# Kernel tuning notes

Measured on AMD Instinct MI355X. Metric: run time of the kernel, lower is better.

The kernel has to match this reference:

```python
import jax, jax.numpy as jnp
import numpy as np
import math

B, L, D, H, R = 2, 1024, 768, 12, 256
DH = D // H  # 64


def layernorm(x, g, b, eps=1e-5):
    mu = jnp.mean(x, axis=-1, keepdims=True)
    var = jnp.mean((x - mu) ** 2, axis=-1, keepdims=True)
    return (x - mu) / jnp.sqrt(var + eps) * g + b


def setup_inputs() -> dict:
    key = jax.random.key(0)
    ks = jax.random.split(key, 8)
    x = jax.random.normal(ks[0], (B, L, D), dtype=jnp.float32)
    conv_w = jax.random.normal(ks[1], (D, 3), dtype=jnp.float32) * 0.3   # depthwise k=3
    conv_b = jnp.zeros((D,), jnp.float32)
    ln_g = jnp.ones((D,), jnp.float32)
    ln_b = jnp.zeros((D,), jnp.float32)
    qkv_w = jax.random.normal(ks[2], (3 * D, D), dtype=jnp.float32) / math.sqrt(D)
    qkv_b = jnp.zeros((3 * D,), jnp.float32)
    bn_w1 = jax.random.normal(ks[3], (R, D), dtype=jnp.float32) / math.sqrt(D)
    bn_w2 = jax.random.normal(ks[4], (H * 5, R), dtype=jnp.float32) / math.sqrt(R)
    temperature = jnp.ones((1,), jnp.float32) * 0.5
    proj_w = jax.random.normal(ks[5], (D, D), dtype=jnp.float32) / math.sqrt(D)
    proj_b = jnp.zeros((D,), jnp.float32)
    mn_g = jnp.ones((DH,), jnp.float32)
    mn_b = jnp.zeros((DH,), jnp.float32)
    return {"x": x, "conv_w": conv_w, "conv_b": conv_b, "ln_g": ln_g, "ln_b": ln_b,
            "qkv_w": qkv_w, "qkv_b": qkv_b, "bn_w1": bn_w1, "bn_w2": bn_w2,
            "temperature": temperature, "proj_w": proj_w, "proj_b": proj_b,
            "mn_g": mn_g, "mn_b": mn_b}


def reference(x, conv_w, conv_b, ln_g, ln_b, qkv_w, qkv_b, bn_w1, bn_w2,
              temperature, proj_w, proj_b, mn_g, mn_b):
    Bx, Lx, Dx = x.shape
    # causal depthwise conv1d (kernel 3, pad 2 then drop last 2 == left-pad 2)
    xp = jnp.pad(x, ((0, 0), (2, 0), (0, 0)))
    conv = (xp[:, 0:Lx] * conv_w[:, 0] + xp[:, 1:Lx + 1] * conv_w[:, 1]
            + xp[:, 2:Lx + 2] * conv_w[:, 2]) + conv_b
    x_conv = x + conv
    xn = layernorm(x_conv, ln_g, ln_b)

    qkv = xn @ qkv_w.T + qkv_b
    q, k, v = jnp.split(qkv, 3, axis=-1)

    params = (jax.nn.silu(xn @ bn_w1.T) @ bn_w2.T).reshape(Bx, Lx, H, 5)
    sem_amp = jax.nn.sigmoid(params[..., 0])
    sem_phase = jnp.tanh(params[..., 1]) * math.pi
    ctx_amp = jax.nn.sigmoid(params[..., 2])
    ctx_phase = jnp.tanh(params[..., 3]) * math.pi
    decay = 0.3 + 0.65 * jax.nn.sigmoid(params[..., 4])  # (B,L,H)
    gate = jax.nn.sigmoid(sem_amp * ctx_amp * jnp.cos(sem_phase - ctx_phase) * temperature[0])

    q_f = (jax.nn.elu(q) + 1.0).reshape(Bx, Lx, H, DH)
    k_f = (jax.nn.elu(k) + 1.0).reshape(Bx, Lx, H, DH)
    v_f = v.reshape(Bx, Lx, H, DH)

    one_minus = 1.0 - decay                                    # (B,L,H)
    kv_input = jnp.einsum('blhd,blhe->blhde', k_f, v_f)        # (B,L,H,dh,dh)
    kv_input = jnp.clip(kv_input * (gate * one_minus)[..., None, None], -5.0, 5.0)

    df = jnp.exp(jnp.cumsum(jnp.log(decay), axis=1))           # (B,L,H)
    safe_df = df + 1e-8
    kv_states = jnp.cumsum(kv_input / safe_df[..., None, None], axis=1) * df[..., None, None]

    z = jnp.cumsum(k_f * one_minus[..., None] / safe_df[..., None], axis=1) * df[..., None]
    z = jnp.clip(z, -10000.0, 10000.0)

    out_num = jnp.einsum('blhd,blhde->blhe', q_f, kv_states)   # (B,L,H,dh)
    den = jnp.sum(q_f * z, axis=-1, keepdims=True) + 0.0001
    out = layernorm(out_num / den, mn_g, mn_b)                 # (B,L,H,dh)

    y = out.reshape(Bx, Lx, Dx) @ proj_w.T + proj_b
    return y, gate
```

## Files before the change

kernel.cpp:

```cpp
#include <hip/hip_runtime.h>
#include <math.h>

#define LL 1024
#define DD 768
#define HH 12
#define CL 16
#define NC 64
#define NBH 24

typedef __bf16 bf16x8 __attribute__((ext_vector_type(8)));
typedef __bf16 bf16x4 __attribute__((ext_vector_type(4)));
typedef float floatx4 __attribute__((ext_vector_type(4)));

typedef const void __attribute__((address_space(1)))* gas_ptr;
typedef void __attribute__((address_space(3)))* las_ptr;

__device__ __forceinline__ void gl_lds16(const void* g, void* s) {
  __builtin_amdgcn_global_load_lds((gas_ptr)g, (las_ptr)s, 16, 0, 0);
}

__device__ __forceinline__ float wave_sum64(float v) {
#pragma unroll
  for (int off = 32; off; off >>= 1) v += __shfl_xor(v, off, 64);
  return v;
}

__device__ __forceinline__ float sigm(float x) { return 1.0f / (1.0f + expf(-x)); }

__global__ __launch_bounds__(256) void convert_all(
    const float* __restrict__ qkvw, const float* __restrict__ bnw1,
    const float* __restrict__ projw, const float* __restrict__ w2,
    __bf16* __restrict__ dq, __bf16* __restrict__ d1,
    __bf16* __restrict__ dp, __bf16* __restrict__ dw2) {
  int i = blockIdx.x * 256 + threadIdx.x;
  if (i >= 647168) return;
  if (i >= 638976) {
    int off = i - 638976;
    bf16x4 o;
    if (off < 3840) {
      float4 v = ((const float4*)w2)[off];
      o[0] = (__bf16)v.x; o[1] = (__bf16)v.y; o[2] = (__bf16)v.z; o[3] = (__bf16)v.w;
    } else {
      o[0] = (__bf16)0.f; o[1] = (__bf16)0.f; o[2] = (__bf16)0.f; o[3] = (__bf16)0.f;
    }
    ((bf16x4*)dw2)[off] = o;
    return;
  }
  const float* s; __bf16* d; int off;
  if (i < 442368)      { s = qkvw;  d = dq; off = i; }
  else if (i < 491520) { s = bnw1;  d = d1; off = i - 442368; }
  else                 { s = projw; d = dp; off = i - 491520; }
  float4 v = ((const float4*)s)[off];
  bf16x4 o;
  o[0] = (__bf16)v.x; o[1] = (__bf16)v.y; o[2] = (__bf16)v.z; o[3] = (__bf16)v.w;
  ((bf16x4*)d)[off] = o;
}

__global__ __launch_bounds__(256) void conv_ln_kernel(
    const float* __restrict__ x, const float* __restrict__ cw,
    const float* __restrict__ cb, const float* __restrict__ g,
    const float* __restrict__ bta, __bf16* __restrict__ xn) {
  int row = blockIdx.x;
  int l = row & (LL - 1);
  const float* xr = x + (size_t)row * DD;
  __shared__ float red[16];
  float vals[3];
  float s = 0.f, ss = 0.f;
#pragma unroll
  for (int i = 0; i < 3; i++) {
    int d = threadIdx.x + i * 256;
    float x0 = xr[d];
    float xm1 = (l >= 1) ? xr[d - DD] : 0.f;
    float xm2 = (l >= 2) ? xr[d - 2 * DD] : 0.f;
    float c = xm2 * cw[d * 3 + 0] + xm1 * cw[d * 3 + 1] + x0 * cw[d * 3 + 2] + cb[d];
    float v = x0 + c;
    vals[i] = v; s += v; ss += v * v;
  }
  s = wave_sum64(s); ss = wave_sum64(ss);
  int wid = threadIdx.x >> 6;
  if ((threadIdx.x & 63) == 0) { red[wid * 2] = s; red[wid * 2 + 1] = ss; }
  __syncthreads();
  if (threadIdx.x == 0) {
    red[8] = red[0] + red[2] + red[4] + red[6];
    red[9] = red[1] + red[3] + red[5] + red[7];
  }
  __syncthreads();
  float mu = red[8] * (1.f / 768.f);
  float var = red[9] * (1.f / 768.f) - mu * mu;
  float inv = rsqrtf(var + 1e-5f);
  __bf16* xo = xn + (size_t)row * DD;
#pragma unroll
  for (int i = 0; i < 3; i++) {
    int d = threadIdx.x + i * 256;
    xo[d] = (__bf16)((vals[i] - mu) * inv * g[d] + bta[d]);
  }
}

template <int BM, int MODE, bool HASBIAS, bool OUTBF>
__global__ __launch_bounds__(256) void gemm_mfma_kernel(
    const __bf16* __restrict__ A, const __bf16* __restrict__ Bw,
    const float* __restrict__ bias, void* __restrict__ Cv,
    int M, int N, int K) {
  constexpr int MI = BM / 32;
  __shared__ __attribute__((aligned(16))) __bf16 As[BM * 64];
  __shared__ __attribute__((aligned(16))) __bf16 Bs[128 * 64];
  int m0 = blockIdx.y * BM, n0 = blockIdx.x * 128;
  int tid = threadIdx.x;
  int w = tid >> 6, lane = tid & 63;
  int wm = w >> 1, wn = w & 1;
  int quad = lane >> 4, l16 = lane & 15;

  int lrow = lane >> 3;
  int lchunk = (lane & 7) ^ lrow;
  int R0 = w * 8;

  floatx4 acc[MI][4];
#pragma unroll
  for (int i = 0; i < MI; i++)
#pragma unroll
    for (int j = 0; j < 4; j++) acc[i][j] = (floatx4)0.f;

  for (int k0 = 0; k0 < K; k0 += 64) {
    __syncthreads();
#pragma unroll
    for (int r = 0; r < BM / 32; r++) {
      int row = r * 32 + R0 + lrow;
      gl_lds16(A + (size_t)(m0 + row) * K + k0 + lchunk * 8, &As[(r * 32 + R0) * 64]);
    }
#pragma unroll
    for (int r = 0; r < 4; r++) {
      int row = r * 32 + R0 + lrow;
      gl_lds16(Bw + (size_t)(n0 + row) * K + k0 + lchunk * 8, &Bs[(r * 32 + R0) * 64]);
    }
    __syncthreads();
#pragma unroll
    for (int s = 0; s < 2; s++) {
      bf16x8 af[MI], bfr[4];
      int csw = (s << 2) + quad;
#pragma unroll
      for (int i = 0; i < MI; i++) {
        int m = wm * (BM / 2) + i * 16 + l16;
        af[i] = *(const bf16x8*)&As[m * 64 + (csw ^ (l16 & 7)) * 8];
      }
#pragma unroll
      for (int j = 0; j < 4; j++) {
        int n = wn * 64 + j * 16 + l16;
        bfr[j] = *(const bf16x8*)&Bs[n * 64 + (csw ^ (l16 & 7)) * 8];
      }
#pragma unroll
      for (int i = 0; i < MI; i++)
#pragma unroll
        for (int j = 0; j < 4; j++)
          acc[i][j] = __builtin_amdgcn_mfma_f32_16x16x32_bf16(af[i], bfr[j], acc[i][j], 0, 0, 0);
    }
  }
#pragma unroll
  for (int j = 0; j < 4; j++) {
    int gcol = n0 + wn * 64 + j * 16 + l16;
    float bv = HASBIAS ? bias[gcol] : 0.f;
#pragma unroll
    for (int i = 0; i < MI; i++) {
      int grow = m0 + wm * (BM / 2) + i * 16 + quad * 4;
#pragma unroll
      for (int r = 0; r < 4; r++) {
        float v = acc[i][j][r] + bv;
        if (MODE == 1) { if (gcol < 1536) v = (v > 0.f) ? v + 1.f : expf(v); }
        if (MODE == 2) { v = v / (1.f + expf(-v)); }
        if (OUTBF) ((__bf16*)Cv)[(size_t)(grow + r) * N + gcol] = (__bf16)v;
        else       ((float*)Cv)[(size_t)(grow + r) * N + gcol] = v;
      }
    }
  }
}

__global__ __launch_bounds__(256) void params_df_kernel(
    const float* __restrict__ pp, const float* __restrict__ temp,
    float* __restrict__ gate, float* __restrict__ dec, float* __restrict__ dfb) {
  int bh = blockIdx.x;
  int b = bh / HH, h = bh - b * HH;
  int tid = threadIdx.x;
  int lane = tid & 63, wid = tid >> 6;
  float tv = temp[0];
  const float PI = 3.14159265358979323846f;
  double ls[4];
  double lsum = 0.0;
#pragma unroll
  for (int i = 0; i < 4; i++) {
    int l = tid * 4 + i;
    int row = (b << 10) + l;
    const float* p = pp + (size_t)row * 128 + h * 5;
    float p0 = p[0], p1 = p[1], p2 = p[2], p3 = p[3], p4 = p[4];
    float sa = sigm(p0);
    float sp = tanhf(p1) * PI;
    float ca = sigm(p2);
    float cp = tanhf(p3) * PI;
    float dc = 0.3f + 0.65f * sigm(p4);
    float gt = sigm(sa * ca * cosf(sp - cp) * tv);
    gate[row * HH + h] = gt;
    dec[(bh << 10) + l] = dc;
    lsum += (double)logf(dc);
    ls[i] = lsum;
  }
  double run = lsum;
#pragma unroll
  for (int off = 1; off < 64; off <<= 1) {
    double n = __shfl_up(run, off, 64);
    if (lane >= off) run += n;
  }
  __shared__ double wsum[4];
  if (lane == 63) wsum[wid] = run;
  __syncthreads();
  double wexcl = 0.0;
  for (int k = 0; k < wid; k++) wexcl += wsum[k];
  double excl = wexcl + run - lsum;
  float* dfo = dfb + (bh << 10) + tid * 4;
#pragma unroll
  for (int i = 0; i < 4; i++) dfo[i] = expf((float)(excl + ls[i]));
}

__global__ __launch_bounds__(256) void scan_phase1(
    const float* __restrict__ qkv, const float* __restrict__ dec,
    const float* __restrict__ df, const float* __restrict__ gate,
    float* __restrict__ kvcs, float* __restrict__ zcs, float* __restrict__ Aarr) {
  int blk = blockIdx.x;
  int bh = blk >> 6, c = blk & (NC - 1);
  int b = bh / HH, h = bh - b * HH;
  int tid = threadIdx.x;
  int w = tid >> 6, e = tid & 63;
  int t0 = c * CL;
  __shared__ __attribute__((aligned(16))) float kbuf[CL][64];
  __shared__ __attribute__((aligned(16))) float vbuf[CL][64];
  __shared__ float sbuf[CL][4];
  const float* base = qkv + ((size_t)(b * LL + t0)) * 2304 + h * 64;
  {
    int t = (w << 2) + (e >> 4);
    int col = (e & 15) << 2;
    gl_lds16(base + (size_t)t * 2304 + 768 + col, &kbuf[w << 2][0]);
    gl_lds16(base + (size_t)t * 2304 + 1536 + col, &vbuf[w << 2][0]);
  }
  if (tid < CL) {
    int t = t0 + tid;
    float a = dec[bh * LL + t];
    float d = df[bh * LL + t];
    float r = d / (d + 1e-8f);
    float g = gate[(b * LL + t) * HH + h];
    sbuf[tid][0] = a; sbuf[tid][1] = r; sbuf[tid][2] = g * (1.f - a);
    sbuf[tid][3] = (1.f - a) * r;
  }
  __syncthreads();
  float KV[16];
#pragma unroll
  for (int d = 0; d < 16; d++) KV[d] = 0.f;
  float z = 0.f, A = 1.f;
  for (int t = 0; t < CL; t++) {
    float a = sbuf[t][0], r = sbuf[t][1], cs = sbuf[t][2], w1r = sbuf[t][3];
    float vc = vbuf[t][e] * cs;
    A *= a;
#pragma unroll
    for (int d4 = 0; d4 < 4; d4++) {
      float4 k4 = *(const float4*)&kbuf[t][(w << 4) + (d4 << 2)];
      float kr[4] = {k4.x, k4.y, k4.z, k4.w};
#pragma unroll
      for (int j = 0; j < 4; j++) {
        float u = fminf(fmaxf(kr[j] * vc, -5.f), 5.f);
        KV[(d4 << 2) + j] = fmaf(a, KV[(d4 << 2) + j], r * u);
      }
    }
    z = fmaf(a, z, kbuf[t][e] * w1r);
  }
  float* kvo = kvcs + (size_t)blk * 4096 + (w << 4) * 64 + e;
#pragma unroll
  for (int d = 0; d < 16; d++) kvo[d * 64] = KV[d];
  if (w == 0) zcs[blk * 64 + e] = z;
  if (tid == 0) Aarr[blk] = A;
}

__global__ __launch_bounds__(256) void combine_kernel(
    const float* __restrict__ Aarr, float* __restrict__ kv, float* __restrict__ z) {
  int g = blockIdx.x * 256 + threadIdx.x;
  if (g < NBH * 4096) {
    int bh = g >> 12, idx = g & 4095;
    const float* Ap = Aarr + bh * NC;
    float* p = kv + (size_t)bh * NC * 4096 + idx;
    float carry = 0.f;
#pragma unroll 8
    for (int c = 0; c < NC; c++) {
      float endv = p[(size_t)c * 4096];
      p[(size_t)c * 4096] = carry;
      carry = fmaf(Ap[c], carry, endv);
    }
  } else {
    int g2 = g - NBH * 4096;
    int bh = g2 >> 6, idx = g2 & 63;
    const float* Ap = Aarr + bh * NC;
    float* p = z + bh * NC * 64 + idx;
    float carry = 0.f;
#pragma unroll 8
    for (int c = 0; c < NC; c++) {
      float endv = p[c * 64];
      p[c * 64] = carry;
      carry = fmaf(Ap[c], carry, endv);
    }
  }
}

__global__ __launch_bounds__(256) void scan_phase3(
    const float* __restrict__ qkv, const float* __restrict__ dec,
    const float* __restrict__ df, const float* __restrict__ gate,
    const float* __restrict__ kvcs, const float* __restrict__ zcs,
    const float* __restrict__ mng, const float* __restrict__ mnb,
    __bf16* __restrict__ att) {
  int blk = blockIdx.x;
  int bh = blk >> 6, c = blk & (NC - 1);
  int b = bh / HH, h = bh - b * HH;
  int tid = threadIdx.x;
  int w = tid >> 6, e = tid & 63;
  int t0 = c * CL;
  __shared__ __attribute__((aligned(16))) float qbuf[CL][64];
  __shared__ __attribute__((aligned(16))) float kbuf[CL][64];
  __shared__ __attribute__((aligned(16))) float vbuf[CL][64];
  __shared__ float sbuf[CL][4];
  __shared__ float pbuf[CL][4][64];
  const float* base = qkv + ((size_t)(b * LL + t0)) * 2304 + h * 64;
  {
    int t = (w << 2) + (e >> 4);
    int col = (e & 15) << 2;
    gl_lds16(base + (size_t)t * 2304 + col, &qbuf[w << 2][0]);
    gl_lds16(base + (size_t)t * 2304 + 768 + col, &kbuf[w << 2][0]);
    gl_lds16(base + (size_t)t * 2304 + 1536 + col, &vbuf[w << 2][0]);
  }
  if (tid < CL) {
    int t = t0 + tid;
    float a = dec[bh * LL + t];
    float d = df[bh * LL + t];
    float r = d / (d + 1e-8f);
    float g = gate[(b * LL + t) * HH + h];
    sbuf[tid][0] = a; sbuf[tid][1] = r; sbuf[tid][2] = g * (1.f - a);
    sbuf[tid][3] = (1.f - a) * r;
  }
  float KV[16];
  const float* kvi = kvcs + (size_t)blk * 4096 + (w << 4) * 64 + e;
#pragma unroll
  for (int d = 0; d < 16; d++) KV[d] = kvi[d * 64];
  float z = zcs[blk * 64 + e];
  float zsnap[4];
  __syncthreads();
  for (int t = 0; t < CL; t++) {
    float a = sbuf[t][0], r = sbuf[t][1], cs = sbuf[t][2], w1r = sbuf[t][3];
    float vc = vbuf[t][e] * cs;
    float onp = 0.f;
#pragma unroll
    for (int d4 = 0; d4 < 4; d4++) {
      float4 k4 = *(const float4*)&kbuf[t][(w << 4) + (d4 << 2)];
      float4 q4 = *(const float4*)&qbuf[t][(w << 4) + (d4 << 2)];
      float kr[4] = {k4.x, k4.y, k4.z, k4.w};
      float qr[4] = {q4.x, q4.y, q4.z, q4.w};
#pragma unroll
      for (int j = 0; j < 4; j++) {
        float u = fminf(fmaxf(kr[j] * vc, -5.f), 5.f);
        float nv = fmaf(a, KV[(d4 << 2) + j], r * u);
        KV[(d4 << 2) + j] = nv;
        onp = fmaf(qr[j], nv, onp);
      }
    }
    pbuf[t][w][e] = onp;
    z = fmaf(a, z, kbuf[t][e] * w1r);
    if ((t >> 2) == w) zsnap[t & 3] = z;
  }
  __syncthreads();
  float mg = mng[e], mb = mnb[e];
#pragma unroll
  for (int i = 0; i < 4; i++) {
    int t = (w << 2) + i;
    float on = pbuf[t][0][e] + pbuf[t][1][e] + pbuf[t][2][e] + pbuf[t][3][e];
    float zc = fminf(fmaxf(zsnap[i], -10000.f), 10000.f);
    float qe = qbuf[t][e];
    float s0 = qe * zc, s1 = on, s2 = on * on;
#pragma unroll
    for (int off = 32; off; off >>= 1) {
      s0 += __shfl_xor(s0, off, 64);
      s1 += __shfl_xor(s1, off, 64);
      s2 += __shfl_xor(s2, off, 64);
    }
    float den = s0 + 1e-4f;
    float idn = 1.f / den;
    float o = on * idn;
    float mu = s1 * idn * (1.f / 64.f);
    float E2 = s2 * idn * idn * (1.f / 64.f);
    float var = E2 - mu * mu;
    float outv = (o - mu) * rsqrtf(var + 1e-5f) * mg + mb;
    att[((size_t)(b * LL + t0 + t)) * DD + h * 64 + e] = (__bf16)outv;
  }
}

extern "C" void kernel_launch(void* const* d_in, const int* in_sizes, int n_in,
                              void* d_out, int out_size, void* d_ws, size_t ws_size,
                              hipStream_t stream) {
  (void)in_sizes; (void)n_in; (void)out_size; (void)ws_size;
  const float* x           = (const float*)d_in[0];
  const float* conv_w      = (const float*)d_in[1];
  const float* conv_b      = (const float*)d_in[2];
  const float* ln_g        = (const float*)d_in[3];
  const float* ln_b        = (const float*)d_in[4];
  const float* qkv_w       = (const float*)d_in[5];
  const float* qkv_b       = (const float*)d_in[6];
  const float* bn_w1       = (const float*)d_in[7];
  const float* bn_w2       = (const float*)d_in[8];
  const float* temperature = (const float*)d_in[9];
  const float* proj_w      = (const float*)d_in[10];
  const float* proj_b      = (const float*)d_in[11];
  const float* mn_g        = (const float*)d_in[12];
  const float* mn_b        = (const float*)d_in[13];

  float* y    = (float*)d_out;
  float* gate = y + 2 * 1024 * 768;

  char* ws = (char*)d_ws;
  __bf16* xn_bf   = (__bf16*)(ws);
  __bf16* att_bf  = xn_bf;
  float*  qkva    = (float*)(ws + 3145728);
  __bf16* hbuf_bf = (__bf16*)(ws + 22020096);
  float*  pp      = (float*)(ws + 23068672);
  float*  dec     = (float*)(ws + 24117248);
  float*  dfb     = (float*)(ws + 24215552);
  float*  kvcs    = (float*)(ws + 24313856);
  __bf16* qkvw_bf = (__bf16*)(ws + 24313856);
  float*  zcs     = (float*)(ws + 49479680);
  float*  Aarr    = (float*)(ws + 49872896);
  __bf16* bnw1_bf = (__bf16*)(ws + 49879040);
  __bf16* projw_bf= (__bf16*)(ws + 50272256);
  __bf16* w2p_bf  = (__bf16*)(ws + 51451904);

  convert_all<<<2528, 256, 0, stream>>>(qkv_w, bn_w1, proj_w, bn_w2,
                                        qkvw_bf, bnw1_bf, projw_bf, w2p_bf);

  conv_ln_kernel<<<2048, 256, 0, stream>>>(x, conv_w, conv_b, ln_g, ln_b, xn_bf);

  gemm_mfma_kernel<64, 1, true, false><<<dim3(18, 32), 256, 0, stream>>>(
      xn_bf, qkvw_bf, qkv_b, qkva, 2048, 2304, 768);

  gemm_mfma_kernel<64, 2, false, true><<<dim3(2, 32), 256, 0, stream>>>(
      xn_bf, bnw1_bf, nullptr, hbuf_bf, 2048, 256, 768);

  gemm_mfma_kernel<64, 0, false, false><<<dim3(1, 32), 256, 0, stream>>>(
      hbuf_bf, w2p_bf, nullptr, pp, 2048, 128, 256);

  params_df_kernel<<<NBH, 256, 0, stream>>>(pp, temperature, gate, dec, dfb);

  scan_phase1<<<NBH * NC, 256, 0, stream>>>(qkva, dec, dfb, gate, kvcs, zcs, Aarr);

  combine_kernel<<<390, 256, 0, stream>>>(Aarr, kvcs, zcs);

  scan_phase3<<<NBH * NC, 256, 0, stream>>>(qkva, dec, dfb, gate, kvcs, zcs,
                                            mn_g, mn_b, att_bf);

  gemm_mfma_kernel<64, 0, true, false><<<dim3(6, 32), 256, 0, stream>>>(
      att_bf, projw_bf, proj_b, y, 2048, 768, 768);
}
```

Baseline: 193.7 us.

## Fuse weight conversion with conv+LN, merge QKV and bottleneck GEMMs, bf16 chunk states

Merges the weight-conversion and conv+layernorm kernels into one launch, and concatenates the qkv and bn_w1 weights so a single GEMM produces both the qkv activations and the SiLU bottleneck hidden. The per-chunk KV carry states are stored in bf16 instead of fp32, which halves the traffic through the combine pass. Clamps now use fmed3. The aim is fewer launches and less memory traffic, at the cost of reduced precision in the inter-chunk state carry.

```diff
diff --git a/kernel.cpp b/kernel.cpp
--- a/kernel.cpp
+++ b/kernel.cpp
@@ -26,40 +26,42 @@
 }
 
 __device__ __forceinline__ float sigm(float x) { return 1.0f / (1.0f + expf(-x)); }
-
-__global__ __launch_bounds__(256) void convert_all(
+__device__ __forceinline__ float clamp5(float x) {
+  return __builtin_amdgcn_fmed3f(x, -5.f, 5.f);
+}
+
+__global__ __launch_bounds__(256) void prep_kernel(
+    const float* __restrict__ x, const float* __restrict__ cw,
+    const float* __restrict__ cb, const float* __restrict__ g,
+    const float* __restrict__ bta, __bf16* __restrict__ xn,
     const float* __restrict__ qkvw, const float* __restrict__ bnw1,
     const float* __restrict__ projw, const float* __restrict__ w2,
-    __bf16* __restrict__ dq, __bf16* __restrict__ d1,
-    __bf16* __restrict__ dp, __bf16* __restrict__ dw2) {
-  int i = blockIdx.x * 256 + threadIdx.x;
-  if (i >= 647168) return;
-  if (i >= 638976) {
-    int off = i - 638976;
+    __bf16* __restrict__ wqb, __bf16* __restrict__ dp, __bf16* __restrict__ dw2) {
+  if (blockIdx.x >= 2048) {
+    int i = (blockIdx.x - 2048) * 256 + threadIdx.x;
+    if (i >= 647168) return;
     bf16x4 o;
-    if (off < 3840) {
-      float4 v = ((const float4*)w2)[off];
-      o[0] = (__bf16)v.x; o[1] = (__bf16)v.y; o[2] = (__bf16)v.z; o[3] = (__bf16)v.w;
-    } else {
-      o[0] = (__bf16)0.f; o[1] = (__bf16)0.f; o[2] = (__bf16)0.f; o[3] = (__bf16)0.f;
-    }
-    ((bf16x4*)dw2)[off] = o;
+    if (i >= 638976) {
+      int off = i - 638976;
+      if (off < 3840) {
+        float4 v = ((const float4*)w2)[off];
+        o[0] = (__bf16)v.x; o[1] = (__bf16)v.y; o[2] = (__bf16)v.z; o[3] = (__bf16)v.w;
+      } else {
+        o[0] = (__bf16)0.f; o[1] = (__bf16)0.f; o[2] = (__bf16)0.f; o[3] = (__bf16)0.f;
+      }
+      ((bf16x4*)dw2)[off] = o;
+      return;
+    }
+    const float* s; __bf16* d; int off;
+    if (i < 442368)      { s = qkvw;  d = wqb;  off = i; }
+    else if (i < 491520) { s = bnw1;  d = wqb;  off = i; }
+    else                 { s = projw; d = dp;   off = i - 491520; }
+    int soff = (i < 442368) ? i : (i < 491520 ? i - 442368 : off);
+    float4 v = ((const float4*)s)[soff];
+    o[0] = (__bf16)v.x; o[1] = (__bf16)v.y; o[2] = (__bf16)v.z; o[3] = (__bf16)v.w;
+    ((bf16x4*)d)[off] = o;
     return;
   }
-  const float* s; __bf16* d; int off;
-  if (i < 442368)      { s = qkvw;  d = dq; off = i; }
-  else if (i < 491520) { s = bnw1;  d = d1; off = i - 442368; }
-  else                 { s = projw; d = dp; off = i - 491520; }
-  float4 v = ((const float4*)s)[off];
-  bf16x4 o;
-  o[0] = (__bf16)v.x; o[1] = (__bf16)v.y; o[2] = (__bf16)v.z; o[3] = (__bf16)v.w;
-  ((bf16x4*)d)[off] = o;
-}
-
-__global__ __launch_bounds__(256) void conv_ln_kernel(
-    const float* __restrict__ x, const float* __restrict__ cw,
-    const float* __restrict__ cb, const float* __restrict__ g,
-    const float* __restrict__ bta, __bf16* __restrict__ xn) {
   int row = blockIdx.x;
   int l = row & (LL - 1);
   const float* xr = x + (size_t)row * DD;
@@ -99,7 +101,7 @@
 template <int BM, int MODE, bool HASBIAS, bool OUTBF>
 __global__ __launch_bounds__(256) void gemm_mfma_kernel(
     const __bf16* __restrict__ A, const __bf16* __restrict__ Bw,
-    const float* __restrict__ bias, void* __restrict__ Cv,
+    const float* __restrict__ bias, void* __restrict__ Cv, void* __restrict__ C2,
     int M, int N, int K) {
   constexpr int MI = BM / 32;
   __shared__ __attribute__((aligned(16))) __bf16 As[BM * 64];
@@ -157,17 +159,44 @@
 #pragma unroll
   for (int j = 0; j < 4; j++) {
     int gcol = n0 + wn * 64 + j * 16 + l16;
-    float bv = HASBIAS ? bias[gcol] : 0.f;
-#pragma unroll
-    for (int i = 0; i < MI; i++) {
-      int grow = m0 + wm * (BM / 2) + i * 16 + quad * 4;
-#pragma unroll
-      for (int r = 0; r < 4; r++) {
-        float v = acc[i][j][r] + bv;
-        if (MODE == 1) { if (gcol < 1536) v = (v > 0.f) ? v + 1.f : expf(v); }
-        if (MODE == 2) { v = v / (1.f + expf(-v)); }
-        if (OUTBF) ((__bf16*)Cv)[(size_t)(grow + r) * N + gcol] = (__bf16)v;
-        else       ((float*)Cv)[(size_t)(grow + r) * N + gcol] = v;
+    if (MODE == 3) {
+      if (gcol < 2304) {
+        float bv = bias[gcol];
+        bool isqk = gcol < 1536;
+#pragma unroll
+        for (int i = 0; i < MI; i++) {
+          int grow = m0 + wm * (BM / 2) + i * 16 + quad * 4;
+#pragma unroll
+          for (int r = 0; r < 4; r++) {
+            float v = acc[i][j][r] + bv;
+            if (isqk) v = (v > 0.f) ? v + 1.f : expf(v);
+            ((float*)Cv)[(size_t)(grow + r) * 2304 + gcol] = v;
+          }
+        }
+      } else {
+        int hcol = gcol - 2304;
+#pragma unroll
+        for (int i = 0; i < MI; i++) {
+          int grow = m0 + wm * (BM / 2) + i * 16 + quad * 4;
+#pragma unroll
+          for (int r = 0; r < 4; r++) {
+            float v = acc[i][j][r];
+            v = v / (1.f + expf(-v));
+            ((__bf16*)C2)[(size_t)(grow + r) * 256 + hcol] = (__bf16)v;
+          }
+        }
+      }
+    } else {
+      float bv = HASBIAS ? bias[gcol] : 0.f;
+#pragma unroll
+      for (int i = 0; i < MI; i++) {
+        int grow = m0 + wm * (BM / 2) + i * 16 + quad * 4;
+#pragma unroll
+        for (int r = 0; r < 4; r++) {
+          float v = acc[i][j][r] + bv;
+          if (OUTBF) ((__bf16*)Cv)[(size_t)(grow + r) * N + gcol] = (__bf16)v;
+          else       ((float*)Cv)[(size_t)(grow + r) * N + gcol] = v;
+        }
       }
     }
   }
@@ -221,7 +250,7 @@
 __global__ __launch_bounds__(256) void scan_phase1(
     const float* __restrict__ qkv, const float* __restrict__ dec,
     const float* __restrict__ df, const float* __restrict__ gate,
-    float* __restrict__ kvcs, float* __restrict__ zcs, float* __restrict__ Aarr) {
+    __bf16* __restrict__ kvcs, float* __restrict__ zcs, float* __restrict__ Aarr) {
   int blk = blockIdx.x;
   int bh = blk >> 6, c = blk & (NC - 1);
   int b = bh / HH, h = bh - b * HH;
@@ -262,35 +291,36 @@
       float kr[4] = {k4.x, k4.y, k4.z, k4.w};
 #pragma unroll
       for (int j = 0; j < 4; j++) {
-        float u = fminf(fmaxf(kr[j] * vc, -5.f), 5.f);
+        float u = clamp5(kr[j] * vc);
         KV[(d4 << 2) + j] = fmaf(a, KV[(d4 << 2) + j], r * u);
       }
     }
     z = fmaf(a, z, kbuf[t][e] * w1r);
   }
-  float* kvo = kvcs + (size_t)blk * 4096 + (w << 4) * 64 + e;
-#pragma unroll
-  for (int d = 0; d < 16; d++) kvo[d * 64] = KV[d];
+  __bf16* kvo = kvcs + (size_t)blk * 4096 + (w << 4) * 64 + e;
+#pragma unroll
+  for (int d = 0; d < 16; d++) kvo[d * 64] = (__bf16)KV[d];
   if (w == 0) zcs[blk * 64 + e] = z;
   if (tid == 0) Aarr[blk] = A;
 }
 
 __global__ __launch_bounds__(256) void combine_kernel(
-    const float* __restrict__ Aarr, float* __restrict__ kv, float* __restrict__ z) {
+    const float* __restrict__ Aarr, __bf16* __restrict__ kv, float* __restrict__ z) {
   int g = blockIdx.x * 256 + threadIdx.x;
   if (g < NBH * 4096) {
     int bh = g >> 12, idx = g & 4095;
     const float* Ap = Aarr + bh * NC;
-    float* p = kv + (size_t)bh * NC * 4096 + idx;
+    __bf16* p = kv + (size_t)bh * NC * 4096 + idx;
     float carry = 0.f;
 #pragma unroll 8
     for (int c = 0; c < NC; c++) {
-      float endv = p[(size_t)c * 4096];
-      p[(size_t)c * 4096] = carry;
+      float endv = (float)p[(size_t)c * 4096];
+      p[(size_t)c * 4096] = (__bf16)carry;
       carry = fmaf(Ap[c], carry, endv);
     }
   } else {
     int g2 = g - NBH * 4096;
+    if (g2 >= NBH * 64) return;
     int bh = g2 >> 6, idx = g2 & 63;
     const float* Ap = Aarr + bh * NC;
     float* p = z + bh * NC * 64 + idx;
@@ -307,7 +337,7 @@
 __global__ __launch_bounds__(256) void scan_phase3(
     const float* __restrict__ qkv, const float* __restrict__ dec,
     const float* __restrict__ df, const float* __restrict__ gate,
-    const float* __restrict__ kvcs, const float* __restrict__ zcs,
+    const __bf16* __restrict__ kvcs, const float* __restrict__ zcs,
     const float* __restrict__ mng, const float* __restrict__ mnb,
     __bf16* __restrict__ att) {
   int blk = blockIdx.x;
@@ -339,9 +369,9 @@
     sbuf[tid][3] = (1.f - a) * r;
   }
   float KV[16];
-  const float* kvi = kvcs + (size_t)blk * 4096 + (w << 4) * 64 + e;
-#pragma unroll
-  for (int d = 0; d < 16; d++) KV[d] = kvi[d * 64];
+  const __bf16* kvi = kvcs + (size_t)blk * 4096 + (w << 4) * 64 + e;
+#pragma unroll
+  for (int d = 0; d < 16; d++) KV[d] = (float)kvi[d * 64];
   float z = zcs[blk * 64 + e];
   float zsnap[4];
   __syncthreads();
@@ -357,7 +387,7 @@
       float qr[4] = {q4.x, q4.y, q4.z, q4.w};
 #pragma unroll
       for (int j = 0; j < 4; j++) {
-        float u = fminf(fmaxf(kr[j] * vc, -5.f), 5.f);
+        float u = clamp5(kr[j] * vc);
         float nv = fmaf(a, KV[(d4 << 2) + j], r * u);
         KV[(d4 << 2) + j] = nv;
         onp = fmaf(qr[j], nv, onp);
@@ -373,7 +403,7 @@
   for (int i = 0; i < 4; i++) {
     int t = (w << 2) + i;
     float on = pbuf[t][0][e] + pbuf[t][1][e] + pbuf[t][2][e] + pbuf[t][3][e];
-    float zc = fminf(fmaxf(zsnap[i], -10000.f), 10000.f);
+    float zc = __builtin_amdgcn_fmed3f(zsnap[i], -10000.f, 10000.f);
     float qe = qbuf[t][e];
     float s0 = qe * zc, s1 = on, s2 = on * on;
 #pragma unroll
@@ -423,27 +453,22 @@
   float*  pp      = (float*)(ws + 23068672);
   float*  dec     = (float*)(ws + 24117248);
   float*  dfb     = (float*)(ws + 24215552);
-  float*  kvcs    = (float*)(ws + 24313856);
-  __bf16* qkvw_bf = (__bf16*)(ws + 24313856);
-  float*  zcs     = (float*)(ws + 49479680);
-  float*  Aarr    = (float*)(ws + 49872896);
-  __bf16* bnw1_bf = (__bf16*)(ws + 49879040);
-  __bf16* projw_bf= (__bf16*)(ws + 50272256);
-  __bf16* w2p_bf  = (__bf16*)(ws + 51451904);
-
-  convert_all<<<2528, 256, 0, stream>>>(qkv_w, bn_w1, proj_w, bn_w2,
-                                        qkvw_bf, bnw1_bf, projw_bf, w2p_bf);
-
-  conv_ln_kernel<<<2048, 256, 0, stream>>>(x, conv_w, conv_b, ln_g, ln_b, xn_bf);
-
-  gemm_mfma_kernel<64, 1, true, false><<<dim3(18, 32), 256, 0, stream>>>(
-      xn_bf, qkvw_bf, qkv_b, qkva, 2048, 2304, 768);
-
-  gemm_mfma_kernel<64, 2, false, true><<<dim3(2, 32), 256, 0, stream>>>(
-      xn_bf, bnw1_bf, nullptr, hbuf_bf, 2048, 256, 768);
+  __bf16* kvcs    = (__bf16*)(ws + 24313856);
+  __bf16* wqb_bf  = (__bf16*)(ws + 24313856);
+  float*  zcs     = (float*)(ws + 36896768);
+  float*  Aarr    = (float*)(ws + 37289984);
+  __bf16* projw_bf= (__bf16*)(ws + 37296128);
+  __bf16* w2p_bf  = (__bf16*)(ws + 38475776);
+
+  prep_kernel<<<4576, 256, 0, stream>>>(x, conv_w, conv_b, ln_g, ln_b, xn_bf,
+                                        qkv_w, bn_w1, proj_w, bn_w2,
+                                        wqb_bf, projw_bf, w2p_bf);
+
+  gemm_mfma_kernel<64, 3, true, false><<<dim3(20, 32), 256, 0, stream>>>(
+      xn_bf, wqb_bf, qkv_b, qkva, hbuf_bf, 2048, 2560, 768);
 
   gemm_mfma_kernel<64, 0, false, false><<<dim3(1, 32), 256, 0, stream>>>(
-      hbuf_bf, w2p_bf, nullptr, pp, 2048, 128, 256);
+      hbuf_bf, w2p_bf, nullptr, pp, nullptr, 2048, 128, 256);
 
   params_df_kernel<<<NBH, 256, 0, stream>>>(pp, temperature, gate, dec, dfb);
 
@@ -455,5 +480,5 @@
                                             mn_g, mn_b, att_bf);
 
   gemm_mfma_kernel<64, 0, true, false><<<dim3(6, 32), 256, 0, stream>>>(
-      att_bf, projw_bf, proj_b, y, 2048, 768, 768);
-}
+      att_bf, projw_bf, proj_b, y, nullptr, 2048, 768, 768);
+}
```

New measurement: 176.1 us. -9.1%, faster.
